# Kernel optimization log

Hardware: AMD Instinct MI355X
Metric: run time of the kernel (lower is better)

Reference implementation:

```python
import jax, jax.numpy as jnp
import numpy as np

B, V, E, K, H = 8, 4096, 256, 6, 8
HD = E // H  # head dim = 32


def _knn_idx(x, k):
    # brute-force squared-euclidean KNN (pytorch3d knn_points, return_sorted=True)
    sq = jnp.sum(x * x, axis=-1)                      # [B, V]
    d2 = sq[:, :, None] + sq[:, None, :] - 2.0 * jnp.einsum('bie,bje->bij', x, x)  # [B,V,V]
    _, idx = jax.lax.top_k(-d2, k)                    # ascending distance -> [B, V, K]
    return idx


def setup_inputs() -> dict:
    key = jax.random.key(0)
    kx, kq, kk, kv, ko = jax.random.split(key, 5)
    s = 1.0 / np.sqrt(E)
    return {
        'x':  jax.random.normal(kx, (B, V, E), dtype=jnp.float32),
        'Wq': jax.random.normal(kq, (E, E), dtype=jnp.float32) * s,
        'Wk': jax.random.normal(kk, (E, E), dtype=jnp.float32) * s,
        'Wv': jax.random.normal(kv, (E, E), dtype=jnp.float32) * s,
        'Wo': jax.random.normal(ko, (E, E), dtype=jnp.float32) * s,
    }


def reference(x, Wq, Wk, Wv, Wo):
    idx = _knn_idx(x, K)                                   # [B, V, K] int32
    k = jax.vmap(lambda xb, ib: xb[ib])(x, idx)            # gather -> [B, V, K, E]
    v = k - x[:, :, None, :]                               # use_direction: v = k - q

    # per-point 1-query / K-key multihead attention (bias-free, eval mode)
    scale = 1.0 / np.sqrt(HD)
    qh = (x @ Wq.T).reshape(B, V, H, HD)                   # [B,V,H,HD]
    kh = jnp.einsum('bvke,fe->bvkf', k, Wk).reshape(B, V, K, H, HD)
    vh = jnp.einsum('bvke,fe->bvkf', v, Wv).reshape(B, V, K, H, HD)
    scores = jnp.einsum('bvhd,bvkhd->bvhk', qh, kh) * scale  # [B,V,H,K]
    attn = jax.nn.softmax(scores, axis=-1)
    out = jnp.einsum('bvhk,bvkhd->bvhd', attn, vh).reshape(B, V, E) @ Wo.T

    # attention weights averaged over heads, scatter-added onto neighbor ids
    x_w = jnp.mean(attn, axis=2)                            # [B, V, K]
    x_w = jax.vmap(lambda i, w: jnp.zeros((V,), x.dtype).at[i].add(w))(
        idx.reshape(B, -1), x_w.reshape(B, -1))             # [B, V]

    return x + out, x_w
```

## Files before the change

### kernel.cpp

```cpp
#include <hip/hip_runtime.h>
#include <cfloat>
#include <math.h>

#define B_   8
#define V_   4096
#define E_   256
#define K_   6
#define H_   8
#define HD_  32
#define NPTS (B_*V_)

typedef __bf16 bf16x8 __attribute__((ext_vector_type(8)));
typedef float  f32x4  __attribute__((ext_vector_type(4)));
typedef float  f32x16 __attribute__((ext_vector_type(16)));

__device__ __forceinline__ float bf2f(unsigned short u) {
    return __uint_as_float(((unsigned int)u) << 16);
}
__device__ __forceinline__ unsigned short f2bf(float f) {
    unsigned int u = __float_as_uint(f);
    return (unsigned short)((u + 0x7fffu + ((u >> 16) & 1u)) >> 16);
}
__device__ __forceinline__ unsigned int med3u(unsigned int a, unsigned int b,
                                              unsigned int c) {
    unsigned int d;
    asm("v_med3_u32 %0, %1, %2, %3" : "=v"(d) : "v"(a), "v"(b), "v"(c));
    return d;
}
__device__ __forceinline__ void push6(unsigned int (&k6)[6], unsigned int key) {
    k6[5] = med3u(k6[4], k6[5], key);
    k6[4] = med3u(k6[3], k6[4], key);
    k6[3] = med3u(k6[2], k6[3], key);
    k6[2] = med3u(k6[1], k6[2], key);
    k6[1] = med3u(k6[0], k6[1], key);
    k6[0] = min(k6[0], key);
}
__device__ __forceinline__ unsigned int bfscale2(unsigned int u) {
    return (u + 0x05000500u) ^ 0x80008000u;
}

__global__ __launch_bounds__(256) void cvtsq_kernel(const float* __restrict__ x,
                                                    const float* __restrict__ Wq,
                                                    const float* __restrict__ Wk,
                                                    const float* __restrict__ Wv,
                                                    const float* __restrict__ Wo,
                                                    unsigned short* __restrict__ xh,
                                                    unsigned short* __restrict__ Wh,
                                                    float* __restrict__ sqp,
                                                    float* __restrict__ xw) {
    const int bx = blockIdx.x;
    if (bx < 4096) {
        size_t i = ((size_t)bx * 256 + threadIdx.x) * 8;
        float4 a = *reinterpret_cast<const float4*>(x + i);
        float4 b = *reinterpret_cast<const float4*>(x + i + 4);
        ushort o[8] = { f2bf(a.x), f2bf(a.y), f2bf(a.z), f2bf(a.w),
                        f2bf(b.x), f2bf(b.y), f2bf(b.z), f2bf(b.w) };
        *reinterpret_cast<uint4*>(xh + i) = *reinterpret_cast<uint4*>(o);
        float s = a.x*a.x + a.y*a.y + a.z*a.z + a.w*a.w
                + b.x*b.x + b.y*b.y + b.z*b.z + b.w*b.w;
        s += __shfl_xor(s, 1);
        s += __shfl_xor(s, 2);
        s += __shfl_xor(s, 4);
        s += __shfl_xor(s, 8);
        s += __shfl_xor(s, 16);
        if ((threadIdx.x & 31) == 0) {
            int p = bx * 8 + (threadIdx.x >> 5);
            int b_ = p >> 12, col = p & 4095;
            int stripe = col >> 10, cc = col & 1023;
            int t = cc >> 5, rem = cc & 31;
            int h = (rem >> 2) & 1;
            int reg = (rem & 3) | ((rem >> 3) << 2);
            int i2 = (b_ << 12) | (stripe << 10) | (t << 5) | (h << 4) | reg;
            sqp[i2] = (s + 600.f) * 512.f;
        }
    } else {
        const int wb = bx - 4096;
        xw[wb * 256 + threadIdx.x] = 0.f;
        const int m = wb >> 5;
        const float* src = (m == 0) ? Wq : (m == 1) ? Wk : (m == 2) ? Wv : Wo;
        unsigned short* dst = Wh + (size_t)m * 65536;
        size_t i = ((size_t)(wb & 31) * 256 + threadIdx.x) * 8;
        float4 a = *reinterpret_cast<const float4*>(src + i);
        float4 b = *reinterpret_cast<const float4*>(src + i + 4);
        ushort o[8] = { f2bf(a.x), f2bf(a.y), f2bf(a.z), f2bf(a.w),
                        f2bf(b.x), f2bf(b.y), f2bf(b.z), f2bf(b.w) };
        *reinterpret_cast<uint4*>(dst + i) = *reinterpret_cast<uint4*>(o);
    }
}

__global__ __launch_bounds__(256, 2) void knn13_kernel(const unsigned short* __restrict__ xh,
                                                       const float* __restrict__ sqp,
                                                       unsigned int* __restrict__ cand) {
    __shared__ __align__(16) char smem[36864];

    const int b      = blockIdx.z;
    const int row0   = blockIdx.x * 256;
    const int stripe = blockIdx.y;
    const int colbase = stripe * 1024;
    const int tid = threadIdx.x;
    const int w   = tid >> 6;
    const int l   = tid & 63;
    const int ln  = l & 31;
    const int h   = l >> 5;
    const unsigned short* Xb = xh + ((size_t)b << 12) * E_;

    const int myrow0 = row0 + (w << 6) + ln;
    bf16x8 brow0[16], brow1[16];
#pragma unroll
    for (int kg = 0; kg < 16; ++kg) {
        uint4 u0 = *reinterpret_cast<const uint4*>(
            Xb + ((size_t)myrow0 << 8) + kg * 16 + h * 8);
        uint4 u1 = *reinterpret_cast<const uint4*>(
            Xb + ((size_t)(myrow0 + 32) << 8) + kg * 16 + h * 8);
        u0.x = bfscale2(u0.x); u0.y = bfscale2(u0.y);
        u0.z = bfscale2(u0.z); u0.w = bfscale2(u0.w);
        u1.x = bfscale2(u1.x); u1.y = bfscale2(u1.y);
        u1.z = bfscale2(u1.z); u1.w = bfscale2(u1.w);
        brow0[kg] = *reinterpret_cast<bf16x8*>(&u0);
        brow1[kg] = *reinterpret_cast<bf16x8*>(&u1);
    }

    unsigned int bk0[6], bk1[6];
#pragma unroll
    for (int s = 0; s < 6; ++s) { bk0[s] = 0xFFFFFFFFu; bk1[s] = 0xFFFFFFFFu; }

    __builtin_amdgcn_global_load_lds(
        (const __attribute__((address_space(1))) void*)
            (sqp + ((size_t)(b * 4 + stripe) << 10) + tid * 4),
        (__attribute__((address_space(3))) void*)(smem + 32768 + tid * 16), 16, 0, 0);
#pragma unroll
    for (int it = 0; it < 4; ++it) {
        int li = it * 256 + tid, col = li >> 5, sl = li & 31;
        const unsigned short* gp =
            Xb + ((size_t)(colbase + col) << 8) + ((sl ^ (col & 7)) << 3);
        __builtin_amdgcn_global_load_lds(
            (const __attribute__((address_space(1))) void*)gp,
            (__attribute__((address_space(3))) void*)(smem + li * 16), 16, 0, 0);
    }
    __syncthreads();

    for (int t = 0; t < 32; ++t) {
        const int cur = (t & 1) * 16384;
        if (t < 31) {
            char* nbuf = smem + (cur ^ 16384);
            const int c0n = colbase + (t + 1) * 32;
#pragma unroll
            for (int it = 0; it < 4; ++it) {
                int li = it * 256 + tid, col = li >> 5, sl = li & 31;
                const unsigned short* gp =
                    Xb + ((size_t)(c0n + col) << 8) + ((sl ^ (col & 7)) << 3);
                __builtin_amdgcn_global_load_lds(
                    (const __attribute__((address_space(1))) void*)gp,
                    (__attribute__((address_space(3))) void*)(nbuf + li * 16), 16, 0, 0);
            }
        }
        const char* sb = smem + 32768 + t * 128 + h * 64;
        f32x16 acc0;
#pragma unroll
        for (int q = 0; q < 4; ++q) {
            f32x4 sv = *reinterpret_cast<const f32x4*>(sb + q * 16);
            acc0[q * 4 + 0] = sv[0];
            acc0[q * 4 + 1] = sv[1];
            acc0[q * 4 + 2] = sv[2];
            acc0[q * 4 + 3] = sv[3];
        }
        f32x16 acc1 = acc0;

        const char* abase = smem + cur + ln * 512;
        const int swz = (ln & 7);
#pragma unroll
        for (int kg = 0; kg < 16; ++kg) {
            bf16x8 af = *reinterpret_cast<const bf16x8*>(
                abase + ((((kg << 1) + h) ^ swz) << 4));
            acc0 = __builtin_amdgcn_mfma_f32_32x32x16_bf16(af, brow0[kg], acc0, 0, 0, 0);
            acc1 = __builtin_amdgcn_mfma_f32_32x32x16_bf16(af, brow1[kg], acc1, 0, 0, 0);
        }

        const unsigned int cb0 = (unsigned int)(colbase + (t << 5) + (h << 2));
#pragma unroll
        for (int r = 0; r < 16; ++r) {
            unsigned int cidx = cb0 + (r & 3) + ((r >> 2) << 3);
            push6(bk0, ((unsigned int)acc0[r] << 12) | cidx);
            push6(bk1, ((unsigned int)acc1[r] << 12) | cidx);
        }
        __syncthreads();
    }

    size_t p0 = ((size_t)b << 12) + myrow0;
    unsigned int* op0 = cand + p0 * 48 + stripe * 12 + h * 6;
    unsigned int* op1 = cand + (p0 + 32) * 48 + stripe * 12 + h * 6;
#pragma unroll
    for (int s = 0; s < 6; ++s) { op0[s] = bk0[s]; op1[s] = bk1[s]; }
}

__global__ __launch_bounds__(256) void sel_kernel(const unsigned int* __restrict__ cand,
                                                  unsigned short* __restrict__ c16,
                                                  int* __restrict__ idxout,
                                                  unsigned char* __restrict__ flag) {
    int p = blockIdx.x * 256 + threadIdx.x;
    const unsigned int* cp = cand + (size_t)p * 48;
    unsigned int tk[16];
#pragma unroll
    for (int s = 0; s < 16; ++s) tk[s] = 0xFFFFFFFFu;
    for (int j = 0; j < 48; ++j) {
        unsigned int key = cp[j];
#pragma unroll
        for (int s = 15; s > 0; --s) tk[s] = med3u(tk[s - 1], tk[s], key);
        tk[0] = min(tk[0], key);
    }
    unsigned short* op = c16 + (size_t)p * 16;
#pragma unroll
    for (int s = 0; s < 16; ++s) op[s] = (unsigned short)(tk[s] & 4095u);
    int* ip = idxout + (size_t)p * K_;
#pragma unroll
    for (int s = 0; s < 6; ++s) ip[s] = (int)(tk[s] & 4095u);
    float d6 = (float)(tk[5] >> 12) * 0.001953125f;
    float d7 = (float)(tk[6] >> 12) * 0.001953125f;
    flag[p] = (d7 - d6 < 0.4f) ? 1 : 0;
}

__global__ __launch_bounds__(256) void refine_kernel(const float* __restrict__ x,
                                                     const unsigned short* __restrict__ c16,
                                                     const unsigned char* __restrict__ flag,
                                                     int* __restrict__ idxout) {
    int wv = threadIdx.x >> 6;
    int lane = threadIdx.x & 63;
    const int bid = blockIdx.x;
    const int nbk = ((bid & 7) << 10) | (bid >> 3);
    int p = nbk * 4 + wv;
    if (!flag[p]) return;
    int b = p >> 12;
    int vi = p & 4095;
    const float* Xb = x + ((size_t)b << 12) * E_;
    const int half = lane >> 5;
    const int hl = lane & 31;

    double xi[8];
#pragma unroll
    for (int t = 0; t < 8; ++t) xi[t] = (double)Xb[(size_t)vi * E_ + hl + t * 32];

    double bdist[6]; int bidx[6];
#pragma unroll
    for (int s = 0; s < 6; ++s) { bdist[s] = DBL_MAX; bidx[s] = 0x7fffffff; }

    const unsigned short* cp = c16 + (size_t)p * 16;
    for (int c = 0; c < 16; c += 2) {
        int jme = cp[c + half];
        const float* Xj = Xb + (size_t)jme * E_;
        double s = 0.0;
#pragma unroll
        for (int t = 0; t < 8; ++t) {
            double d = xi[t] - (double)Xj[hl + t * 32];
            s = fma(d, d, s);
        }
#pragma unroll
        for (int off = 16; off; off >>= 1) s += __shfl_xor(s, off);
        double sv[2];
        sv[0] = __shfl(s, 0);
        sv[1] = __shfl(s, 32);
        int jv[2] = { (int)cp[c], (int)cp[c + 1] };
#pragma unroll
        for (int q = 0; q < 2; ++q) {
            double sq_ = sv[q]; int j = jv[q];
            if (sq_ < bdist[5] || (sq_ == bdist[5] && j < bidx[5])) {
                bdist[5] = sq_; bidx[5] = j;
#pragma unroll
                for (int t = 5; t > 0; --t) {
                    if (bdist[t] < bdist[t - 1] ||
                        (bdist[t] == bdist[t - 1] && bidx[t] < bidx[t - 1])) {
                        double td = bdist[t]; bdist[t] = bdist[t - 1]; bdist[t - 1] = td;
                        int    ti = bidx[t];  bidx[t]  = bidx[t - 1];  bidx[t - 1]  = ti;
                    } else break;
                }
            }
        }
    }
    if (lane == 0) {
        int* op = idxout + (size_t)p * K_;
#pragma unroll
        for (int s = 0; s < 6; ++s) op[s] = bidx[s];
    }
}

__global__ __launch_bounds__(256, 2) void proj_mfma(const unsigned short* __restrict__ xh,
                                                    const unsigned short* __restrict__ Wh,
                                                    unsigned short* __restrict__ Y) {
    __shared__ __align__(16) char smem[32768];
    const int tid = threadIdx.x;
    const int w = tid >> 6, l = tid & 63, cl = l & 15, g = l >> 4;
    const int row0 = blockIdx.x * 128;
    const int wsel = blockIdx.y;
    const unsigned short* W = Wh + (size_t)wsel * 65536;

    bf16x8 a0[8], a1[8];
    const int ar0 = row0 + (w << 4) + cl;
#pragma unroll
    for (int ks = 0; ks < 8; ++ks) {
        a0[ks] = *reinterpret_cast<const bf16x8*>(xh + ((size_t)ar0 << 8) + ks * 32 + g * 8);
        a1[ks] = *reinterpret_cast<const bf16x8*>(xh + ((size_t)(ar0 + 64) << 8) + ks * 32 + g * 8);
    }

#pragma unroll
    for (int it = 0; it < 4; ++it) {
        int li = it * 256 + tid, col = li >> 5, sl = li & 31;
        const unsigned short* gp = W + ((size_t)col << 8) + ((sl ^ (col & 7)) << 3);
        __builtin_amdgcn_global_load_lds(
            (const __attribute__((address_space(1))) void*)gp,
            (__attribute__((address_space(3))) void*)(smem + li * 16), 16, 0, 0);
    }
    __syncthreads();

    for (int tp = 0; tp < 8; ++tp) {
        const int cur = (tp & 1) * 16384;
        if (tp < 7) {
            char* nbuf = smem + (cur ^ 16384);
            const int colb = (tp + 1) * 32;
#pragma unroll
            for (int it = 0; it < 4; ++it) {
                int li = it * 256 + tid, col = li >> 5, sl = li & 31;
                const unsigned short* gp =
                    W + ((size_t)(colb + col) << 8) + ((sl ^ (col & 7)) << 3);
                __builtin_amdgcn_global_load_lds(
                    (const __attribute__((address_space(1))) void*)gp,
                    (__attribute__((address_space(3))) void*)(nbuf + li * 16), 16, 0, 0);
            }
        }
#pragma unroll
        for (int c01 = 0; c01 < 2; ++c01) {
            const int ct = tp * 2 + c01;
            const int wr = c01 * 16 + cl;
            const char* wbase = smem + cur + wr * 512;
            const int swz = wr & 7;
            f32x4 acc0 = {0.f, 0.f, 0.f, 0.f};
            f32x4 acc1 = {0.f, 0.f, 0.f, 0.f};
#pragma unroll
            for (int ks = 0; ks < 8; ++ks) {
                bf16x8 wf = *reinterpret_cast<const bf16x8*>(
                    wbase + ((((ks << 2) + g) ^ swz) << 4));
                acc0 = __builtin_amdgcn_mfma_f32_16x16x32_bf16(a0[ks], wf, acc0, 0, 0, 0);
                acc1 = __builtin_amdgcn_mfma_f32_16x16x32_bf16(a1[ks], wf, acc1, 0, 0, 0);
            }
#pragma unroll
            for (int r = 0; r < 4; ++r) {
                size_t row = row0 + (w << 4) + (g << 2) + r;
                Y[row * 768 + wsel * 256 + ct * 16 + cl] = f2bf(acc0[r]);
                Y[(row + 64) * 768 + wsel * 256 + ct * 16 + cl] = f2bf(acc1[r]);
            }
        }
        __syncthreads();
    }
}

__global__ __launch_bounds__(256) void attn16_kernel(const unsigned short* __restrict__ Y,
                                                     const int* __restrict__ idx,
                                                     const unsigned short* __restrict__ WoH,
                                                     const float* __restrict__ x,
                                                     float* __restrict__ out,
                                                     float* __restrict__ xw) {
    __shared__ __align__(16) unsigned short P[16][264];
    const int bid = blockIdx.x;
    const int blk = ((bid & 7) << 8) | (bid >> 3);
    const int w = threadIdx.x >> 6;
    const int l = threadIdx.x & 63;
    const int p0 = blk * 16;
    const int b = p0 >> 12;
    const size_t bbase = (size_t)(b << 12) * 768;

    for (int j = 0; j < 4; ++j) {
        const int p = p0 + w * 4 + j;
        const int* ip = idx + (size_t)p * K_;
        int nb[K_];
#pragma unroll
        for (int k = 0; k < K_; ++k) nb[k] = ip[k];

        const unsigned short* Yp = Y + (size_t)p * 768;
        ushort4 q4 = *reinterpret_cast<const ushort4*>(Yp + l * 4);
        ushort4 s4 = *reinterpret_cast<const ushort4*>(Yp + 512 + l * 4);
        float q0 = bf2f(q4.x), q1 = bf2f(q4.y), q2 = bf2f(q4.z), q3 = bf2f(q4.w);
        float v0 = bf2f(s4.x), v1 = bf2f(s4.y), v2 = bf2f(s4.z), v3 = bf2f(s4.w);

        float sc[K_];
#pragma unroll
        for (int k = 0; k < K_; ++k) {
            ushort4 k4 = *reinterpret_cast<const ushort4*>(
                Y + bbase + (size_t)nb[k] * 768 + 256 + l * 4);
            float s = q0 * bf2f(k4.x) + q1 * bf2f(k4.y)
                    + q2 * bf2f(k4.z) + q3 * bf2f(k4.w);
            s += __shfl_xor(s, 1);
            s += __shfl_xor(s, 2);
            s += __shfl_xor(s, 4);
            sc[k] = s * 0.17677669529663687f;
        }
        float m = sc[0];
#pragma unroll
        for (int k = 1; k < K_; ++k) m = fmaxf(m, sc[k]);
        float e[K_], sum = 0.f;
#pragma unroll
        for (int k = 0; k < K_; ++k) { e[k] = __expf(sc[k] - m); sum += e[k]; }
        float inv = 1.f / sum;

        float o0 = 0.f, o1 = 0.f, o2 = 0.f, o3 = 0.f;
        float hs[K_];
#pragma unroll
        for (int k = 0; k < K_; ++k) {
            float a = e[k] * inv;
            ushort4 z4 = *reinterpret_cast<const ushort4*>(
                Y + bbase + (size_t)nb[k] * 768 + 512 + l * 4);
            o0 += a * (bf2f(z4.x) - v0);
            o1 += a * (bf2f(z4.y) - v1);
            o2 += a * (bf2f(z4.z) - v2);
            o3 += a * (bf2f(z4.w) - v3);
            float t = a;
            t += __shfl_xor(t, 8);
            t += __shfl_xor(t, 16);
            t += __shfl_xor(t, 32);
            hs[k] = t * 0.125f;
        }
        ushort o4[4] = { f2bf(o0), f2bf(o1), f2bf(o2), f2bf(o3) };
        *reinterpret_cast<ushort4*>(&P[w * 4 + j][l * 4]) =
            *reinterpret_cast<ushort4*>(o4);
        if (l < K_) atomicAdd(&xw[(b << 12) + nb[l]], hs[l]);
    }
    __syncthreads();

    const int cl = l & 15, g = l >> 4;
    bf16x8 a[8];
#pragma unroll
    for (int ks = 0; ks < 8; ++ks)
        a[ks] = *reinterpret_cast<const bf16x8*>(&P[cl][ks * 32 + g * 8]);

#pragma unroll
    for (int ct = 0; ct < 4; ++ct) {
        const int col0 = w * 64 + ct * 16;
        f32x4 acc = {0.f, 0.f, 0.f, 0.f};
        const unsigned short* Wr = WoH + (size_t)(col0 + cl) * 256 + g * 8;
#pragma unroll
        for (int ks = 0; ks < 8; ++ks) {
            bf16x8 bf = *reinterpret_cast<const bf16x8*>(Wr + ks * 32);
            acc = __builtin_amdgcn_mfma_f32_16x16x32_bf16(a[ks], bf, acc, 0, 0, 0);
        }
#pragma unroll
        for (int r = 0; r < 4; ++r) {
            size_t o = (size_t)(p0 + (g << 2) + r) * E_ + col0 + cl;
            out[o] = acc[r] + x[o];
        }
    }
}

extern "C" void kernel_launch(void* const* d_in, const int* in_sizes, int n_in,
                              void* d_out, int out_size, void* d_ws, size_t ws_size,
                              hipStream_t stream) {
    const float* x  = (const float*)d_in[0];
    const float* Wq = (const float*)d_in[1];
    const float* Wk = (const float*)d_in[2];
    const float* Wv = (const float*)d_in[3];
    const float* Wo = (const float*)d_in[4];

    float* out = (float*)d_out;
    float* xw  = out + (size_t)NPTS * E_;

    char* ws = (char*)d_ws;
    float*          sqpw  = (float*)(ws + 131072);
    unsigned int*   candw = (unsigned int*)(ws + 262144);
    int*            idxw  = (int*)(ws + 6553600);
    unsigned char*  flagw = (unsigned char*)(ws + 7340032);
    unsigned short* Wh    = (unsigned short*)(ws + 7372800);
    unsigned short* c16w  = (unsigned short*)(ws + 7897088);
    unsigned short* Xh    = (unsigned short*)(ws + 8945664);
    unsigned short* Y     = (unsigned short*)(ws + 25722880);

    cvtsq_kernel<<<4096 + 128, 256, 0, stream>>>(x, Wq, Wk, Wv, Wo, Xh, Wh, sqpw, xw);
    knn13_kernel<<<dim3(V_ / 256, 4, B_), 256, 0, stream>>>(Xh, sqpw, candw);
    sel_kernel<<<NPTS / 256, 256, 0, stream>>>(candw, c16w, idxw, flagw);
    refine_kernel<<<NPTS / 4, 256, 0, stream>>>(x, c16w, flagw, idxw);
    proj_mfma<<<dim3(NPTS / 128, 3), 256, 0, stream>>>(Xh, Wh, Y);
    attn16_kernel<<<NPTS / 16, 256, 0, stream>>>(Y, idxw, Wh + 3 * 65536, x, out, xw);
}
```

Measured before the change: 195.3 us.

## Process 32 points per attention block and stage Wo through double-buffered LDS

The attention kernel now handles 32 points per block instead of 16, which halves the number of blocks that each read the full Wo matrix. Wo tiles are streamed into a swizzled, double-buffered LDS region with global_load_lds while the MFMA output projection runs. This is meant to cut redundant global and L2 reads of Wo. In exchange each block uses more LDS and adds per-tile barriers, which may lower occupancy.

```diff
diff --git a/kernel.cpp b/kernel.cpp
--- a/kernel.cpp
+++ b/kernel.cpp
@@ -351,23 +351,26 @@
     }
 }
 
-__global__ __launch_bounds__(256) void attn16_kernel(const unsigned short* __restrict__ Y,
+__global__ __launch_bounds__(256) void attn32_kernel(const unsigned short* __restrict__ Y,
                                                      const int* __restrict__ idx,
                                                      const unsigned short* __restrict__ WoH,
                                                      const float* __restrict__ x,
                                                      float* __restrict__ out,
                                                      float* __restrict__ xw) {
-    __shared__ __align__(16) unsigned short P[16][264];
+    __shared__ __align__(16) unsigned short P[32][264];
+    __shared__ __align__(16) char wsmem[32768];
     const int bid = blockIdx.x;
-    const int blk = ((bid & 7) << 8) | (bid >> 3);
-    const int w = threadIdx.x >> 6;
-    const int l = threadIdx.x & 63;
-    const int p0 = blk * 16;
+    const int blk = ((bid & 7) << 7) | (bid >> 3);
+    const int tid = threadIdx.x;
+    const int w = tid >> 6;
+    const int l = tid & 63;
+    const int p0 = blk * 32;
     const int b = p0 >> 12;
     const size_t bbase = (size_t)(b << 12) * 768;
 
-    for (int j = 0; j < 4; ++j) {
-        const int p = p0 + w * 4 + j;
+    for (int j = 0; j < 8; ++j) {
+        const int pr = w * 8 + j;
+        const int p = p0 + pr;
         const int* ip = idx + (size_t)p * K_;
         int nb[K_];
 #pragma unroll
@@ -417,33 +420,61 @@
             hs[k] = t * 0.125f;
         }
         ushort o4[4] = { f2bf(o0), f2bf(o1), f2bf(o2), f2bf(o3) };
-        *reinterpret_cast<ushort4*>(&P[w * 4 + j][l * 4]) =
-            *reinterpret_cast<ushort4*>(o4);
+        *reinterpret_cast<ushort4*>(&P[pr][l * 4]) = *reinterpret_cast<ushort4*>(o4);
         if (l < K_) atomicAdd(&xw[(b << 12) + nb[l]], hs[l]);
     }
     __syncthreads();
 
     const int cl = l & 15, g = l >> 4;
+    const int p16 = (w & 1) << 4;
+    const int cth = w >> 1;
     bf16x8 a[8];
 #pragma unroll
     for (int ks = 0; ks < 8; ++ks)
-        a[ks] = *reinterpret_cast<const bf16x8*>(&P[cl][ks * 32 + g * 8]);
-
-#pragma unroll
-    for (int ct = 0; ct < 4; ++ct) {
-        const int col0 = w * 64 + ct * 16;
+        a[ks] = *reinterpret_cast<const bf16x8*>(&P[p16 + cl][ks * 32 + g * 8]);
+
+#pragma unroll
+    for (int it = 0; it < 4; ++it) {
+        int li = it * 256 + tid, row = li >> 5, sl = li & 31;
+        const unsigned short* gp = WoH + ((size_t)row << 8) + ((sl ^ (row & 7)) << 3);
+        __builtin_amdgcn_global_load_lds(
+            (const __attribute__((address_space(1))) void*)gp,
+            (__attribute__((address_space(3))) void*)(wsmem + li * 16), 16, 0, 0);
+    }
+    __syncthreads();
+
+    for (int tp = 0; tp < 8; ++tp) {
+        const int cur = (tp & 1) * 16384;
+        if (tp < 7) {
+            char* nbuf = wsmem + (cur ^ 16384);
+            const int rowb = (tp + 1) * 32;
+#pragma unroll
+            for (int it = 0; it < 4; ++it) {
+                int li = it * 256 + tid, row = li >> 5, sl = li & 31;
+                const unsigned short* gp =
+                    WoH + ((size_t)(rowb + row) << 8) + ((sl ^ (row & 7)) << 3);
+                __builtin_amdgcn_global_load_lds(
+                    (const __attribute__((address_space(1))) void*)gp,
+                    (__attribute__((address_space(3))) void*)(nbuf + li * 16), 16, 0, 0);
+            }
+        }
+        const int ct = tp * 2 + cth;
+        const int wr = cth * 16 + cl;
+        const char* wbase = wsmem + cur + wr * 512;
+        const int swz = wr & 7;
         f32x4 acc = {0.f, 0.f, 0.f, 0.f};
-        const unsigned short* Wr = WoH + (size_t)(col0 + cl) * 256 + g * 8;
 #pragma unroll
         for (int ks = 0; ks < 8; ++ks) {
-            bf16x8 bf = *reinterpret_cast<const bf16x8*>(Wr + ks * 32);
-            acc = __builtin_amdgcn_mfma_f32_16x16x32_bf16(a[ks], bf, acc, 0, 0, 0);
+            bf16x8 wf = *reinterpret_cast<const bf16x8*>(
+                wbase + ((((ks << 2) + g) ^ swz) << 4));
+            acc = __builtin_amdgcn_mfma_f32_16x16x32_bf16(a[ks], wf, acc, 0, 0, 0);
         }
 #pragma unroll
         for (int r = 0; r < 4; ++r) {
-            size_t o = (size_t)(p0 + (g << 2) + r) * E_ + col0 + cl;
+            size_t o = (size_t)(p0 + p16 + (g << 2) + r) * E_ + ct * 16 + cl;
             out[o] = acc[r] + x[o];
         }
+        __syncthreads();
     }
 }
 
@@ -474,5 +505,5 @@
     sel_kernel<<<NPTS / 256, 256, 0, stream>>>(candw, c16w, idxw, flagw);
     refine_kernel<<<NPTS / 4, 256, 0, stream>>>(x, c16w, flagw, idxw);
     proj_mfma<<<dim3(NPTS / 128, 3), 256, 0, stream>>>(Xh, Wh, Y);
-    attn16_kernel<<<NPTS / 16, 256, 0, stream>>>(Y, idxw, Wh + 3 * 65536, x, out, xw);
-}
+    attn32_kernel<<<NPTS / 32, 256, 0, stream>>>(Y, idxw, Wh + 3 * 65536, x, out, xw);
+}
```

New measurement: 184.0 us, median of 2. 1.06x faster.
